# Optimization experiments

Measured on AMD Instinct MI355X. Metric: run time of the kernel, lower is better.

## Reference

```python
import jax, jax.numpy as jnp
import numpy as np

B, N, IN, HID, OUT, H = 8, 1024, 64, 64, 64, 4


def dense_gat(x, adj, W, a_src, a_dst, bias, heads):
    # x: [B,N,Fin], adj: [B,N,N] (0/1, self-loops already set), W: [heads*C, Fin]
    b, n, _ = x.shape
    c = W.shape[0] // heads
    h = (x @ W.T).reshape(b, n, heads, c)                      # [B,N,H,C]
    s = jnp.einsum('bnhc,hc->bnh', h, a_src)                   # source scores
    d = jnp.einsum('bnhc,hc->bnh', h, a_dst)                   # dest scores
    # alpha[b,i,j,h] = s[b,j,h] + d[b,i,h]
    alpha = s[:, None, :, :] + d[:, :, None, :]                # [B,N,N,H]
    alpha = jax.nn.leaky_relu(alpha, 0.2)
    alpha = jnp.where(adj[..., None] > 0, alpha, jnp.float32(-1e9))
    alpha = jax.nn.softmax(alpha, axis=2)                      # softmax over neighbors j
    out = jnp.einsum('bijh,bjhc->bihc', alpha, h)              # [B,N,H,C]
    return out.reshape(b, n, heads * c) + bias


def setup_inputs() -> dict:
    key = jax.random.key(0)
    ks = jax.random.split(key, 24)
    rn = lambda k, shape: (jax.random.normal(k, shape, jnp.float32) * 0.05)
    node_features = jax.random.normal(ks[0], (B, N, IN), jnp.float32)
    adj = jax.random.randint(ks[1], (B, N, N), 0, 2, jnp.int32)
    d = dict(
        node_features=node_features, adj=adj,
        w1=rn(ks[2], (H * HID, IN)),  as1=rn(ks[3], (H, HID)), ad1=rn(ks[4], (H, HID)), b1=rn(ks[5], (H * HID,)),
        w2=rn(ks[6], (H * HID, H * HID)), as2=rn(ks[7], (H, HID)), ad2=rn(ks[8], (H, HID)), b2=rn(ks[9], (H * HID,)),
        w3=rn(ks[10], (OUT, H * HID)), as3=rn(ks[11], (1, OUT)), ad3=rn(ks[12], (1, OUT)), b3=rn(ks[13], (OUT,)),
        wn=rn(ks[14], (OUT, OUT)), bn=rn(ks[15], (OUT,)),
        wg=rn(ks[16], (OUT, OUT)), bg=rn(ks[17], (OUT,)),
        wv=rn(ks[18], (1, 2 * OUT)), bv=rn(ks[19], (1,)),
    )
    return d


def reference(node_features, adj, w1, as1, ad1, b1, w2, as2, ad2, b2,
              w3, as3, ad3, b3, wn, bn, wg, bg, wv, bv):
    n = node_features.shape[1]
    adj_sl = jnp.maximum(adj, jnp.eye(n, dtype=adj.dtype)[None])  # add self-loops
    x = jax.nn.relu(dense_gat(node_features, adj_sl, w1, as1, ad1, b1, H))
    x = jax.nn.relu(dense_gat(x, adj_sl, w2, as2, ad2, b2, H))
    x = jax.nn.relu(dense_gat(x, adj_sl, w3, as3, ad3, b3, 1))     # [B,N,OUT]
    g = jnp.broadcast_to(x.sum(axis=-2, keepdims=True), x.shape)   # [B,N,OUT]
    h = jnp.concatenate([x @ wn.T + bn, g @ wg.T + bg], axis=-1)   # [B,N,2*OUT]
    h = jax.nn.relu(h)
    return (h @ wv.T + bv).squeeze(-1)                             # [B,N]
```

## Files before the change

kernel.cpp:

```cpp
#include <hip/hip_runtime.h>
#include <stdint.h>

#define NB 8
#define NN 1024
#define LOG2E 1.44269504088896f

typedef short short8 __attribute__((ext_vector_type(8)));
typedef float floatx4 __attribute__((ext_vector_type(4)));

static __device__ __forceinline__ short f2bf(float x) {
    union { float f; uint32_t u; } v; v.f = x;
    uint32_t r = (v.u + 0x7fffu + ((v.u >> 16) & 1u)) >> 16;
    return (short)r;
}

__global__ __launch_bounds__(256) void prep_all(const int* __restrict__ adj,
        uint64_t* __restrict__ am,
        const float* __restrict__ w1, const float* __restrict__ w2,
        const float* __restrict__ w3, const float* __restrict__ wn,
        ushort* __restrict__ wb1, ushort* __restrict__ wb2,
        ushort* __restrict__ wb3, ushort* __restrict__ wnb,
        float* __restrict__ gsum) {
    if (blockIdx.x < 2048) {
        int wave = blockIdx.x * 4 + (threadIdx.x >> 6);
        int lane = threadIdx.x & 63;
        int b = wave >> 10;
        int i = wave & 1023;
        const int* row = adj + ((size_t)b * NN + i) * NN;
        uint64_t* outp = am + ((size_t)b * NN + i) * 16;
        for (int it = 0; it < 16; ++it) {
            int j = it * 64 + lane;
            int v = (row[j] > 0) || (j == i);
            uint64_t m = __ballot(v);
            if (lane == 0) outp[it] = m;
        }
        return;
    }
    int idx = (blockIdx.x - 2048) * 256 + threadIdx.x;
    const float* src; ushort* dst; int li;
    if (idx < 4096)        { src = w1; dst = wb1; li = idx; }
    else if (idx < 20480)  { src = w2; dst = wb2; li = idx - 4096; }
    else if (idx < 24576)  { src = w3; dst = wb3; li = idx - 20480; }
    else if (idx < 25600)  { src = wn; dst = wnb; li = idx - 24576; }
    else if (idx < 25728) {
        ((float4*)gsum)[idx - 25600] = make_float4(0.f, 0.f, 0.f, 0.f);
        return;
    } else return;
    float4 v = ((const float4*)src)[li];
    ushort4 o;
    o.x = (ushort)f2bf(v.x); o.y = (ushort)f2bf(v.y);
    o.z = (ushort)f2bf(v.z); o.w = (ushort)f2bf(v.w);
    ((ushort4*)dst)[li] = o;
}

template<int K, bool CVT>
__global__ __launch_bounds__(256, 4) void gemm_mfma(const void* __restrict__ Xv,
        const ushort* __restrict__ Wt, ushort* __restrict__ hbF,
        const float* __restrict__ asrc, const float* __restrict__ adst,
        float* __restrict__ s_t, float* __restrict__ d_t, int nheads) {
    __shared__ ushort smem[2][64][88];
    int m0 = blockIdx.x * 64, n0 = blockIdx.y * 64;
    int hd = blockIdx.y;
    int tid = threadIdx.x, w = tid >> 6, L = tid & 63;
    int m15 = L & 15, kq = L >> 4;
    floatx4 acc[4];
#pragma unroll
    for (int ct = 0; ct < 4; ++ct) acc[ct] = (floatx4){0.f, 0.f, 0.f, 0.f};

    for (int k0 = 0; k0 < K; k0 += 64) {
#pragma unroll
        for (int it = 0; it < 2; ++it) {
            int idx = tid + it * 256;
            int r = idx >> 3, sg = idx & 7;
            if (CVT) {
                const float* xf = (const float*)Xv + (size_t)(m0 + r) * K + k0 + sg * 8;
                float4 a0 = *(const float4*)xf, a1 = *(const float4*)(xf + 4);
                ushort t8[8];
                t8[0] = (ushort)f2bf(a0.x); t8[1] = (ushort)f2bf(a0.y);
                t8[2] = (ushort)f2bf(a0.z); t8[3] = (ushort)f2bf(a0.w);
                t8[4] = (ushort)f2bf(a1.x); t8[5] = (ushort)f2bf(a1.y);
                t8[6] = (ushort)f2bf(a1.z); t8[7] = (ushort)f2bf(a1.w);
                *(uint4*)&smem[0][r][sg * 8] = *(uint4*)&t8[0];
            } else {
                const ushort* xs = (const ushort*)Xv + (size_t)(m0 + r) * K + k0 + sg * 8;
                *(uint4*)&smem[0][r][sg * 8] = *(const uint4*)xs;
            }
            *(uint4*)&smem[1][r][sg * 8] = *(const uint4*)&Wt[(size_t)(n0 + r) * K + k0 + sg * 8];
        }
        __syncthreads();
#pragma unroll
        for (int ks = 0; ks < 2; ++ks) {
            short8 a = *(const short8*)&smem[0][16 * w + m15][ks * 32 + kq * 8];
#pragma unroll
            for (int ct = 0; ct < 4; ++ct) {
                short8 bfr = *(const short8*)&smem[1][ct * 16 + m15][ks * 32 + kq * 8];
                acc[ct] = __builtin_amdgcn_mfma_f32_16x16x32_bf16(a, bfr, acc[ct], 0, 0, 0);
            }
        }
        __syncthreads();
    }

    float asv[4], adv[4];
#pragma unroll
    for (int ct = 0; ct < 4; ++ct) {
        asv[ct] = asrc[hd * 64 + ct * 16 + m15];
        adv[ct] = adst[hd * 64 + ct * 16 + m15];
    }
#pragma unroll
    for (int r = 0; r < 4; ++r) {
        float sp = acc[0][r] * asv[0] + acc[1][r] * asv[1] + acc[2][r] * asv[2] + acc[3][r] * asv[3];
        float dp = acc[0][r] * adv[0] + acc[1][r] * adv[1] + acc[2][r] * adv[2] + acc[3][r] * adv[3];
#pragma unroll
        for (int off = 1; off < 16; off <<= 1) {
            sp += __shfl_xor(sp, off);
            dp += __shfl_xor(dp, off);
        }
        if (m15 == 0) {
            int mg = m0 + 16 * w + kq * 4 + r;
            int bb = mg >> 10, node = mg & 1023;
            s_t[((size_t)(bb * nheads + hd)) * NN + node] = sp;
            d_t[((size_t)(bb * nheads + hd)) * NN + node] = dp;
        }
    }

    ushort* tb = (ushort*)smem;
    int jj0 = 16 * w + kq * 4;
    int ks0 = jj0 >> 5, l4 = (jj0 >> 3) & 3, u0 = jj0 & 7;
#pragma unroll
    for (int ct = 0; ct < 4; ++ct) {
        ushort p4[4];
#pragma unroll
        for (int r = 0; r < 4; ++r) p4[r] = (ushort)f2bf(acc[ct][r]);
        *(ushort4*)&tb[(ks0 * 4 + ct) * 512 + (l4 * 16 + m15) * 8 + u0] = *(ushort4*)&p4[0];
    }
    __syncthreads();
    int bb = m0 >> 10, node0 = m0 & 1023, jc = node0 >> 6;
    size_t dstb = ((size_t)(bb * nheads + hd) * 16 + jc) * 4096;
#pragma unroll
    for (int e = 0; e < 2; ++e) {
        int idx = tid + e * 256;
        *(uint4*)&hbF[dstb + (size_t)idx * 8] = *(const uint4*)&tb[idx * 8];
    }
}

__global__ __launch_bounds__(256, 4) void gat_agg_mfma(
        const ushort* __restrict__ hbF, const uint64_t* __restrict__ am,
        const float* __restrict__ s_t, const float* __restrict__ d_t,
        const float* __restrict__ bias, ushort* __restrict__ Xb,
        float* __restrict__ gsum, int nheads, int do_colsum) {
    __shared__ __align__(16) float s_lds[NN];
    __shared__ float red4[4];
    __shared__ __align__(16) float fb[4][17][68];

    int i0 = blockIdx.x * 16;
    int hd = blockIdx.y;
    int b  = blockIdx.z;
    int HC = nheads * 64;
    int tid = threadIdx.x, w = tid >> 6, L = tid & 63;
    int m15 = L & 15, kq = L >> 4;

    const float* srow = s_t + ((size_t)b * nheads + hd) * NN;
    float4 s4 = ((const float4*)srow)[tid];
    *(float4*)&s_lds[tid * 4] = s4;
    float lm = fmaxf(fmaxf(s4.x, s4.y), fmaxf(s4.z, s4.w));
#pragma unroll
    for (int off = 32; off; off >>= 1) lm = fmaxf(lm, __shfl_xor(lm, off));
    if (L == 0) red4[w] = lm;

    const uint64_t* amrow = am + ((size_t)b * NN + i0 + m15) * 16 + w * 4;
    uint64_t aw[4];
    *(uint4*)&aw[0] = *(const uint4*)&amrow[0];
    *(uint4*)&aw[2] = *(const uint4*)&amrow[2];
    float d_i = d_t[((size_t)b * nheads + hd) * NN + i0 + m15];
    __syncthreads();

    float smax = fmaxf(fmaxf(red4[0], red4[1]), fmaxf(red4[2], red4[3]));
    float t0 = smax + d_i;
    float m_up = fmaxf(t0, 0.2f * t0);
    float m2n = -m_up * LOG2E;

    floatx4 acc[4];
#pragma unroll
    for (int ct = 0; ct < 4; ++ct) acc[ct] = (floatx4){0.f, 0.f, 0.f, 0.f};
    float lsum = 0.f;

    const ushort* hs = hbF + (size_t)(b * nheads + hd) * 16 * 4096;
    int wq = w * 4;

    uint4 fr[2][4];
#define LOADG(dst, g) { int t_ = (g) >> 1, ks_ = (g) & 1;                          \
    const ushort* bp = hs + ((size_t)((wq + t_) * 8 + ks_ * 4)) * 512 + (size_t)L * 8; \
    dst[0] = *(const uint4*)bp;            dst[1] = *(const uint4*)(bp + 512);     \
    dst[2] = *(const uint4*)(bp + 1024);   dst[3] = *(const uint4*)(bp + 1536); }

    LOADG(fr[0], 0);
#pragma unroll
    for (int g = 0; g < 8; ++g) {
        if (g < 7) LOADG(fr[(g + 1) & 1], g + 1);
        int t = g >> 1, ks = g & 1;
        int jb = (wq + t) * 64 + ks * 32 + kq * 8;
        float sv[8];
        *(float4*)&sv[0] = *(const float4*)&s_lds[jb];
        *(float4*)&sv[4] = *(const float4*)&s_lds[jb + 4];
        unsigned byte = (unsigned)((aw[t] >> (ks * 32 + kq * 8)) & 0xffull);
        unsigned ue[8];
#pragma unroll
        for (int u = 0; u < 8; ++u) {
            float sc = sv[u] + d_i;
            float lk = fmaxf(sc, 0.2f * sc);
#if __has_builtin(__builtin_amdgcn_exp2f)
            float arg = __builtin_fmaf(lk, LOG2E, m2n);
            arg = ((byte >> u) & 1u) ? arg : -1e30f;
            float e = __builtin_amdgcn_exp2f(arg);
#else
            float e = __expf(fminf(lk + m2n, 0.f));
            e = ((byte >> u) & 1u) ? e : 0.f;
#endif
            lsum += e;
            ue[u] = __float_as_uint(e);
        }
        unsigned pk[4];
#pragma unroll
        for (int k2 = 0; k2 < 4; ++k2)
#if __has_builtin(__builtin_amdgcn_perm)
            pk[k2] = __builtin_amdgcn_perm(ue[2 * k2 + 1], ue[2 * k2], 0x07060302u);
#else
            pk[k2] = (ue[2 * k2] >> 16) | (ue[2 * k2 + 1] & 0xffff0000u);
#endif
        short8 afrag;
        *(uint4*)&afrag = *(uint4*)&pk[0];
#pragma unroll
        for (int ct = 0; ct < 4; ++ct) {
            short8 bfr;
            *(uint4*)&bfr = fr[g & 1][ct];
            acc[ct] = __builtin_amdgcn_mfma_f32_16x16x32_bf16(afrag, bfr, acc[ct], 0, 0, 0);
        }
    }
#undef LOADG

    lsum += __shfl_xor(lsum, 16);
    lsum += __shfl_xor(lsum, 32);

#pragma unroll
    for (int ct = 0; ct < 4; ++ct)
#pragma unroll
        for (int r = 0; r < 4; ++r)
            fb[w][kq * 4 + r][ct * 16 + m15] = acc[ct][r];
    if (kq == 0) fb[w][16][m15] = lsum;
    __syncthreads();

    int rr = tid >> 4, c0 = (tid & 15) * 4;
    float s0 = 0.f, s1 = 0.f, s2 = 0.f, s3 = 0.f, ltot = 0.f;
#pragma unroll
    for (int w2 = 0; w2 < 4; ++w2) {
        float4 a4 = *(const float4*)&fb[w2][rr][c0];
        s0 += a4.x; s1 += a4.y; s2 += a4.z; s3 += a4.w;
        ltot += fb[w2][16][rr];
    }
    float li = 1.f / ltot;
    float4 bv = *(const float4*)&bias[hd * 64 + c0];
    float v0 = fmaxf(s0 * li + bv.x, 0.f);
    float v1 = fmaxf(s1 * li + bv.y, 0.f);
    float v2 = fmaxf(s2 * li + bv.z, 0.f);
    float v3 = fmaxf(s3 * li + bv.w, 0.f);
    ushort4 o;
    o.x = (ushort)f2bf(v0); o.y = (ushort)f2bf(v1);
    o.z = (ushort)f2bf(v2); o.w = (ushort)f2bf(v3);
    *(ushort4*)&Xb[((size_t)(b * NN + i0 + rr)) * HC + hd * 64 + c0] = o;

    if (do_colsum) {
        __syncthreads();
        *(float4*)&fb[0][rr][c0] = make_float4(v0, v1, v2, v3);
        __syncthreads();
        if (tid < 64) {
            float s = 0.f;
#pragma unroll
            for (int r2 = 0; r2 < 16; ++r2) s += fb[0][r2][tid];
            atomicAdd(&gsum[b * 64 + tid], s);
        }
    }
}

__global__ __launch_bounds__(256) void readout_fused(
        const ushort* __restrict__ xb, const ushort* __restrict__ wnb,
        const float* __restrict__ bn, const float* __restrict__ wg,
        const float* __restrict__ bg, const float* __restrict__ wv,
        const float* __restrict__ bv, const float* __restrict__ gsum,
        float* __restrict__ outp) {
    __shared__ ushort xs[64][88];
    __shared__ ushort wns[64][88];
    __shared__ float gcs;
    int b = blockIdx.y, n0 = blockIdx.x * 64;
    int tid = threadIdx.x, w = tid >> 6, L = tid & 63;
    int m15 = L & 15, kq = L >> 4;
#pragma unroll
    for (int it = 0; it < 2; ++it) {
        int idx = tid + it * 256;
        int r = idx >> 3, sg = idx & 7;
        *(uint4*)&xs[r][sg * 8]  = *(const uint4*)&xb[(size_t)(b * NN + n0 + r) * 64 + sg * 8];
        *(uint4*)&wns[r][sg * 8] = *(const uint4*)&wnb[r * 64 + sg * 8];
    }
    if (tid < 64) {
        float acc = bg[tid];
#pragma unroll 8
        for (int c = 0; c < 64; ++c) acc += gsum[b * 64 + c] * wg[tid * 64 + c];
        acc = fmaxf(acc, 0.f) * wv[64 + tid];
#pragma unroll
        for (int off = 32; off; off >>= 1) acc += __shfl_down(acc, off);
        if (tid == 0) gcs = acc + bv[0];
    }
    __syncthreads();

    floatx4 acc[4];
#pragma unroll
    for (int ct = 0; ct < 4; ++ct) acc[ct] = (floatx4){0.f, 0.f, 0.f, 0.f};
#pragma unroll
    for (int ks = 0; ks < 2; ++ks) {
        short8 a = *(const short8*)&xs[16 * w + m15][ks * 32 + kq * 8];
#pragma unroll
        for (int ct = 0; ct < 4; ++ct) {
            short8 bfr = *(const short8*)&wns[ct * 16 + m15][ks * 32 + kq * 8];
            acc[ct] = __builtin_amdgcn_mfma_f32_16x16x32_bf16(a, bfr, acc[ct], 0, 0, 0);
        }
    }
    float bnv[4], wvv[4];
#pragma unroll
    for (int ct = 0; ct < 4; ++ct) {
        bnv[ct] = bn[ct * 16 + m15];
        wvv[ct] = wv[ct * 16 + m15];
    }
    float gc = gcs;
#pragma unroll
    for (int r = 0; r < 4; ++r) {
        float rp = 0.f;
#pragma unroll
        for (int ct = 0; ct < 4; ++ct)
            rp += fmaxf(acc[ct][r] + bnv[ct], 0.f) * wvv[ct];
#pragma unroll
        for (int off = 1; off < 16; off <<= 1) rp += __shfl_xor(rp, off);
        if (m15 == 0)
            outp[(size_t)b * NN + n0 + 16 * w + kq * 4 + r] = rp + gc;
    }
}

extern "C" void kernel_launch(void* const* d_in, const int* in_sizes, int n_in,
                              void* d_out, int out_size, void* d_ws, size_t ws_size,
                              hipStream_t stream) {
    const float* x0  = (const float*)d_in[0];
    const int*   adj = (const int*)  d_in[1];
    const float* w1  = (const float*)d_in[2];
    const float* as1 = (const float*)d_in[3];
    const float* ad1 = (const float*)d_in[4];
    const float* b1  = (const float*)d_in[5];
    const float* w2  = (const float*)d_in[6];
    const float* as2 = (const float*)d_in[7];
    const float* ad2 = (const float*)d_in[8];
    const float* b2  = (const float*)d_in[9];
    const float* w3  = (const float*)d_in[10];
    const float* as3 = (const float*)d_in[11];
    const float* ad3 = (const float*)d_in[12];
    const float* b3  = (const float*)d_in[13];
    const float* wn  = (const float*)d_in[14];
    const float* bn  = (const float*)d_in[15];
    const float* wg  = (const float*)d_in[16];
    const float* bg  = (const float*)d_in[17];
    const float* wv  = (const float*)d_in[18];
    const float* bv  = (const float*)d_in[19];
    float* outp = (float*)d_out;

    char* wsb = (char*)d_ws;
    uint64_t* amask = (uint64_t*)(wsb);
    ushort* hbF  = (ushort*)(wsb + (1u  << 20));
    ushort* xbA  = (ushort*)(wsb + (5u  << 20));
    ushort* xbB  = (ushort*)(wsb + (9u  << 20));
    char* tail   = wsb + (14u << 20);
    float* s_buf = (float*)(tail);
    float* d_buf = (float*)(tail + (1u << 17));
    ushort* wb1  = (ushort*)(tail + (2u << 17));
    ushort* wb2  = (ushort*)(tail + (2u << 17) + (1u << 15));
    ushort* wb3  = (ushort*)(tail + (2u << 17) + (5u << 15));
    ushort* wnb  = (ushort*)(tail + (2u << 17) + (6u << 15));
    float* gsum  = (float*) (tail + (2u << 17) + (6u << 15) + (1u << 13));

    prep_all<<<2149, 256, 0, stream>>>(adj, amask, w1, w2, w3, wn,
                                       wb1, wb2, wb3, wnb, gsum);

    gemm_mfma<64, true><<<dim3(128, 4), 256, 0, stream>>>(x0, wb1, hbF, as1, ad1, s_buf, d_buf, 4);
    gat_agg_mfma<<<dim3(64, 4, 8), 256, 0, stream>>>(hbF, amask, s_buf, d_buf, b1, xbA, gsum, 4, 0);

    gemm_mfma<256, false><<<dim3(128, 4), 256, 0, stream>>>(xbA, wb2, hbF, as2, ad2, s_buf, d_buf, 4);
    gat_agg_mfma<<<dim3(64, 4, 8), 256, 0, stream>>>(hbF, amask, s_buf, d_buf, b2, xbB, gsum, 4, 0);

    gemm_mfma<256, false><<<dim3(128, 1), 256, 0, stream>>>(xbB, wb3, hbF, as3, ad3, s_buf, d_buf, 1);
    gat_agg_mfma<<<dim3(64, 1, 8), 256, 0, stream>>>(hbF, amask, s_buf, d_buf, b3, xbA, gsum, 1, 1);

    readout_fused<<<dim3(16, 8), 256, 0, stream>>>(xbA, wnb, bn, wg, bg, wv, bv, gsum, outp);
}
```

Measured before the change: 179.0 us.

## Process two 16-row groups per block in GAT aggregation to reuse H fragments

The aggregation kernel is templated on a row-group count. For the 4-head layers each block now handles 32 destination rows, so every loaded B-fragment of h and each s_lds read feeds two sets of MFMAs. The goal is to halve global traffic for h per output row and the block count. In exchange it uses more registers (occupancy hint lowered from 4 to 3) and launches half as many blocks; the single-head last layer keeps RG=1.

```diff
diff --git a/kernel.cpp b/kernel.cpp
--- a/kernel.cpp
+++ b/kernel.cpp
@@ -143,16 +143,17 @@
     }
 }
 
-__global__ __launch_bounds__(256, 4) void gat_agg_mfma(
+template<int RG>
+__global__ __launch_bounds__(256, 3) void gat_agg_mfma(
         const ushort* __restrict__ hbF, const uint64_t* __restrict__ am,
         const float* __restrict__ s_t, const float* __restrict__ d_t,
         const float* __restrict__ bias, ushort* __restrict__ Xb,
         float* __restrict__ gsum, int nheads, int do_colsum) {
     __shared__ __align__(16) float s_lds[NN];
     __shared__ float red4[4];
-    __shared__ __align__(16) float fb[4][17][68];
-
-    int i0 = blockIdx.x * 16;
+    __shared__ __align__(16) float fb[4][RG * 17][68];
+
+    int i0 = blockIdx.x * (16 * RG);
     int hd = blockIdx.y;
     int b  = blockIdx.z;
     int HC = nheads * 64;
@@ -167,22 +168,34 @@
     for (int off = 32; off; off >>= 1) lm = fmaxf(lm, __shfl_xor(lm, off));
     if (L == 0) red4[w] = lm;
 
-    const uint64_t* amrow = am + ((size_t)b * NN + i0 + m15) * 16 + w * 4;
-    uint64_t aw[4];
-    *(uint4*)&aw[0] = *(const uint4*)&amrow[0];
-    *(uint4*)&aw[2] = *(const uint4*)&amrow[2];
-    float d_i = d_t[((size_t)b * nheads + hd) * NN + i0 + m15];
+    uint64_t aw[RG][4];
+    float d_i[RG];
+#pragma unroll
+    for (int rg = 0; rg < RG; ++rg) {
+        const uint64_t* amrow = am + ((size_t)b * NN + i0 + rg * 16 + m15) * 16 + w * 4;
+        *(uint4*)&aw[rg][0] = *(const uint4*)&amrow[0];
+        *(uint4*)&aw[rg][2] = *(const uint4*)&amrow[2];
+        d_i[rg] = d_t[((size_t)b * nheads + hd) * NN + i0 + rg * 16 + m15];
+    }
     __syncthreads();
 
     float smax = fmaxf(fmaxf(red4[0], red4[1]), fmaxf(red4[2], red4[3]));
-    float t0 = smax + d_i;
-    float m_up = fmaxf(t0, 0.2f * t0);
-    float m2n = -m_up * LOG2E;
-
-    floatx4 acc[4];
-#pragma unroll
-    for (int ct = 0; ct < 4; ++ct) acc[ct] = (floatx4){0.f, 0.f, 0.f, 0.f};
-    float lsum = 0.f;
+    float m2n[RG];
+#pragma unroll
+    for (int rg = 0; rg < RG; ++rg) {
+        float t0 = smax + d_i[rg];
+        float m_up = fmaxf(t0, 0.2f * t0);
+        m2n[rg] = -m_up * LOG2E;
+    }
+
+    floatx4 acc[4][RG];
+#pragma unroll
+    for (int ct = 0; ct < 4; ++ct)
+#pragma unroll
+        for (int rg = 0; rg < RG; ++rg) acc[ct][rg] = (floatx4){0.f, 0.f, 0.f, 0.f};
+    float lsum[RG];
+#pragma unroll
+    for (int rg = 0; rg < RG; ++rg) lsum[rg] = 0.f;
 
     const ushort* hs = hbF + (size_t)(b * nheads + hd) * 16 * 4096;
     int wq = w * 4;
@@ -202,81 +215,111 @@
         float sv[8];
         *(float4*)&sv[0] = *(const float4*)&s_lds[jb];
         *(float4*)&sv[4] = *(const float4*)&s_lds[jb + 4];
-        unsigned byte = (unsigned)((aw[t] >> (ks * 32 + kq * 8)) & 0xffull);
-        unsigned ue[8];
-#pragma unroll
-        for (int u = 0; u < 8; ++u) {
-            float sc = sv[u] + d_i;
-            float lk = fmaxf(sc, 0.2f * sc);
+#pragma unroll
+        for (int rg = 0; rg < RG; ++rg) {
+            unsigned byte = (unsigned)((aw[rg][t] >> (ks * 32 + kq * 8)) & 0xffull);
+            unsigned ue[8];
+#pragma unroll
+            for (int u = 0; u < 8; ++u) {
+                float sc = sv[u] + d_i[rg];
+                float lk = fmaxf(sc, 0.2f * sc);
 #if __has_builtin(__builtin_amdgcn_exp2f)
-            float arg = __builtin_fmaf(lk, LOG2E, m2n);
-            arg = ((byte >> u) & 1u) ? arg : -1e30f;
-            float e = __builtin_amdgcn_exp2f(arg);
+                float arg = __builtin_fmaf(lk, LOG2E, m2n[rg]);
+                arg = ((byte >> u) & 1u) ? arg : -1e30f;
+                float e = __builtin_amdgcn_exp2f(arg);
 #else
-            float e = __expf(fminf(lk + m2n, 0.f));
-            e = ((byte >> u) & 1u) ? e : 0.f;
+                float e = __expf(fminf(lk + m2n[rg], 0.f));
+                e = ((byte >> u) & 1u) ? e : 0.f;
 #endif
-            lsum += e;
-            ue[u] = __float_as_uint(e);
-        }
-        unsigned pk[4];
-#pragma unroll
-        for (int k2 = 0; k2 < 4; ++k2)
+                lsum[rg] += e;
+                ue[u] = __float_as_uint(e);
+            }
+            unsigned pk[4];
+#pragma unroll
+            for (int k2 = 0; k2 < 4; ++k2)
 #if __has_builtin(__builtin_amdgcn_perm)
-            pk[k2] = __builtin_amdgcn_perm(ue[2 * k2 + 1], ue[2 * k2], 0x07060302u);
+                pk[k2] = __builtin_amdgcn_perm(ue[2 * k2 + 1], ue[2 * k2], 0x07060302u);
 #else
-            pk[k2] = (ue[2 * k2] >> 16) | (ue[2 * k2 + 1] & 0xffff0000u);
+                pk[k2] = (ue[2 * k2] >> 16) | (ue[2 * k2 + 1] & 0xffff0000u);
 #endif
-        short8 afrag;
-        *(uint4*)&afrag = *(uint4*)&pk[0];
-#pragma unroll
-        for (int ct = 0; ct < 4; ++ct) {
-            short8 bfr;
-            *(uint4*)&bfr = fr[g & 1][ct];
-            acc[ct] = __builtin_amdgcn_mfma_f32_16x16x32_bf16(afrag, bfr, acc[ct], 0, 0, 0);
+            short8 afrag;
+            *(uint4*)&afrag = *(uint4*)&pk[0];
+#pragma unroll
+            for (int ct = 0; ct < 4; ++ct) {
+                short8 bfr;
+                *(uint4*)&bfr = fr[g & 1][ct];
+                acc[ct][rg] = __builtin_amdgcn_mfma_f32_16x16x32_bf16(afrag, bfr, acc[ct][rg], 0, 0, 0);
+            }
         }
     }
 #undef LOADG
 
-    lsum += __shfl_xor(lsum, 16);
-    lsum += __shfl_xor(lsum, 32);
-
-#pragma unroll
-    for (int ct = 0; ct < 4; ++ct)
-#pragma unroll
-        for (int r = 0; r < 4; ++r)
-            fb[w][kq * 4 + r][ct * 16 + m15] = acc[ct][r];
-    if (kq == 0) fb[w][16][m15] = lsum;
+#pragma unroll
+    for (int rg = 0; rg < RG; ++rg) {
+        lsum[rg] += __shfl_xor(lsum[rg], 16);
+        lsum[rg] += __shfl_xor(lsum[rg], 32);
+        if (kq == 0) fb[w][rg * 17 + 16][m15] = lsum[rg];
+#pragma unroll
+        for (int ct = 0; ct < 4; ++ct)
+#pragma unroll
+            for (int r = 0; r < 4; ++r)
+                fb[w][rg * 17 + kq * 4 + r][ct * 16 + m15] = acc[ct][rg][r];
+    }
     __syncthreads();
 
-    int rr = tid >> 4, c0 = (tid & 15) * 4;
-    float s0 = 0.f, s1 = 0.f, s2 = 0.f, s3 = 0.f, ltot = 0.f;
-#pragma unroll
-    for (int w2 = 0; w2 < 4; ++w2) {
-        float4 a4 = *(const float4*)&fb[w2][rr][c0];
-        s0 += a4.x; s1 += a4.y; s2 += a4.z; s3 += a4.w;
-        ltot += fb[w2][16][rr];
-    }
-    float li = 1.f / ltot;
-    float4 bv = *(const float4*)&bias[hd * 64 + c0];
-    float v0 = fmaxf(s0 * li + bv.x, 0.f);
-    float v1 = fmaxf(s1 * li + bv.y, 0.f);
-    float v2 = fmaxf(s2 * li + bv.z, 0.f);
-    float v3 = fmaxf(s3 * li + bv.w, 0.f);
-    ushort4 o;
-    o.x = (ushort)f2bf(v0); o.y = (ushort)f2bf(v1);
-    o.z = (ushort)f2bf(v2); o.w = (ushort)f2bf(v3);
-    *(ushort4*)&Xb[((size_t)(b * NN + i0 + rr)) * HC + hd * 64 + c0] = o;
-
-    if (do_colsum) {
-        __syncthreads();
-        *(float4*)&fb[0][rr][c0] = make_float4(v0, v1, v2, v3);
-        __syncthreads();
-        if (tid < 64) {
-            float s = 0.f;
-#pragma unroll
-            for (int r2 = 0; r2 < 16; ++r2) s += fb[0][r2][tid];
-            atomicAdd(&gsum[b * 64 + tid], s);
+    if (RG == 2) {
+        int rr = tid >> 3, c0 = (tid & 7) * 8;
+        int g2 = rr >> 4, ri = rr & 15;
+        float s0[8];
+#pragma unroll
+        for (int k2 = 0; k2 < 8; ++k2) s0[k2] = 0.f;
+        float ltot = 0.f;
+#pragma unroll
+        for (int w2 = 0; w2 < 4; ++w2) {
+            float4 a4 = *(const float4*)&fb[w2][g2 * 17 + ri][c0];
+            float4 b4 = *(const float4*)&fb[w2][g2 * 17 + ri][c0 + 4];
+            s0[0] += a4.x; s0[1] += a4.y; s0[2] += a4.z; s0[3] += a4.w;
+            s0[4] += b4.x; s0[5] += b4.y; s0[6] += b4.z; s0[7] += b4.w;
+            ltot += fb[w2][g2 * 17 + 16][ri];
+        }
+        float li = 1.f / ltot;
+        float4 bv0 = *(const float4*)&bias[hd * 64 + c0];
+        float4 bv1 = *(const float4*)&bias[hd * 64 + c0 + 4];
+        float bvv[8] = {bv0.x, bv0.y, bv0.z, bv0.w, bv1.x, bv1.y, bv1.z, bv1.w};
+        ushort o[8];
+#pragma unroll
+        for (int k2 = 0; k2 < 8; ++k2)
+            o[k2] = (ushort)f2bf(fmaxf(s0[k2] * li + bvv[k2], 0.f));
+        *(uint4*)&Xb[((size_t)(b * NN + i0 + rr)) * HC + hd * 64 + c0] = *(uint4*)&o[0];
+    } else {
+        int rr = tid >> 4, c0 = (tid & 15) * 4;
+        float s0 = 0.f, s1 = 0.f, s2 = 0.f, s3 = 0.f, ltot = 0.f;
+#pragma unroll
+        for (int w2 = 0; w2 < 4; ++w2) {
+            float4 a4 = *(const float4*)&fb[w2][rr][c0];
+            s0 += a4.x; s1 += a4.y; s2 += a4.z; s3 += a4.w;
+            ltot += fb[w2][16][rr];
+        }
+        float li = 1.f / ltot;
+        float4 bv = *(const float4*)&bias[hd * 64 + c0];
+        float v0 = fmaxf(s0 * li + bv.x, 0.f);
+        float v1 = fmaxf(s1 * li + bv.y, 0.f);
+        float v2 = fmaxf(s2 * li + bv.z, 0.f);
+        float v3 = fmaxf(s3 * li + bv.w, 0.f);
+        ushort4 o;
+        o.x = (ushort)f2bf(v0); o.y = (ushort)f2bf(v1);
+        o.z = (ushort)f2bf(v2); o.w = (ushort)f2bf(v3);
+        *(ushort4*)&Xb[((size_t)(b * NN + i0 + rr)) * HC + hd * 64 + c0] = o;
+        if (do_colsum) {
+            __syncthreads();
+            *(float4*)&fb[0][rr][c0] = make_float4(v0, v1, v2, v3);
+            __syncthreads();
+            if (tid < 64) {
+                float s = 0.f;
+#pragma unroll
+                for (int r2 = 0; r2 < 16; ++r2) s += fb[0][r2][tid];
+                atomicAdd(&gsum[b * 64 + tid], s);
+            }
         }
     }
 }
@@ -386,13 +429,13 @@
                                        wb1, wb2, wb3, wnb, gsum);
 
     gemm_mfma<64, true><<<dim3(128, 4), 256, 0, stream>>>(x0, wb1, hbF, as1, ad1, s_buf, d_buf, 4);
-    gat_agg_mfma<<<dim3(64, 4, 8), 256, 0, stream>>>(hbF, amask, s_buf, d_buf, b1, xbA, gsum, 4, 0);
+    gat_agg_mfma<2><<<dim3(32, 4, 8), 256, 0, stream>>>(hbF, amask, s_buf, d_buf, b1, xbA, gsum, 4, 0);
 
     gemm_mfma<256, false><<<dim3(128, 4), 256, 0, stream>>>(xbA, wb2, hbF, as2, ad2, s_buf, d_buf, 4);
-    gat_agg_mfma<<<dim3(64, 4, 8), 256, 0, stream>>>(hbF, amask, s_buf, d_buf, b2, xbB, gsum, 4, 0);
+    gat_agg_mfma<2><<<dim3(32, 4, 8), 256, 0, stream>>>(hbF, amask, s_buf, d_buf, b2, xbB, gsum, 4, 0);
 
     gemm_mfma<256, false><<<dim3(128, 1), 256, 0, stream>>>(xbB, wb3, hbF, as3, ad3, s_buf, d_buf, 1);
-    gat_agg_mfma<<<dim3(64, 1, 8), 256, 0, stream>>>(hbF, amask, s_buf, d_buf, b3, xbA, gsum, 1, 1);
+    gat_agg_mfma<1><<<dim3(64, 1, 8), 256, 0, stream>>>(hbF, amask, s_buf, d_buf, b3, xbA, gsum, 1, 1);
 
     readout_fused<<<dim3(16, 8), 256, 0, stream>>>(xbA, wnb, bn, wg, bg, wv, bv, gsum, outp);
 }
```

Measured after the change: 180.8 us. Within noise of the previous version (+1.0%).
